# Kernel optimization log

Measured on AMD Instinct MI355X. Metric: run time of the kernel, lower is better.

The kernel has to match this reference:

```python
import jax, jax.numpy as jnp
import numpy as np
from jax import lax

RADIUS = 4
SIGMA_1 = 5.0
SIGMA_2 = 1.0


def _gaussian_kernel_3d(radius, sigma):
    x = np.linspace(-radius, radius, 2 * radius + 1)
    xx, yy, zz = np.meshgrid(x, x, x)
    dist2 = xx ** 2 + yy ** 2 + zz ** 2
    k = np.exp(-dist2 / (2.0 * sigma ** 2)).astype(np.float32)
    return jnp.asarray(k)[None, None]  # [O=1, I=1, D, H, W]


def _conv3d_same(x, kernel, radius):
    # x: [B,1,D,H,W], kernel: [1,1,kd,kh,kw]
    pad = [(radius, radius)] * 3
    return lax.conv_general_dilated(
        x, kernel, window_strides=(1, 1, 1), padding=pad,
        dimension_numbers=('NCDHW', 'OIDHW', 'NCDHW'))


def setup_inputs() -> dict:
    key = jax.random.key(0)
    k1, k2 = jax.random.split(key)
    labels = jax.random.uniform(k1, (4, 1, 160, 160, 160), dtype=jnp.float32)
    inputs = jax.random.uniform(k2, (4, 1, 160, 160, 160), dtype=jnp.float32)
    return {"labels": labels, "inputs": inputs}


def reference(labels, inputs):
    kernel = _gaussian_kernel_3d(RADIUS, SIGMA_1)
    num_classes = 2
    p0 = labels[:, 0:1]  # [B,1,D,H,W]
    loss = jnp.float32(0.0)
    for k in range(num_classes):
        class_probs = p0 if k == 0 else 1.0 - p0
        class_mean = (jnp.mean(inputs * class_probs, axis=(2, 3, 4), keepdims=True)
                      / (jnp.mean(class_probs, axis=(2, 3, 4), keepdims=True) + 1e-5))
        diff = jnp.sum((inputs - class_mean) ** 2, axis=1, keepdims=True)  # [B,1,D,H,W]
        weights = jnp.exp(-(diff ** 2) / (SIGMA_2 ** 2))
        numerator = jnp.sum(class_probs * _conv3d_same(class_probs * weights, kernel, RADIUS))
        denominator = jnp.sum(class_probs * _conv3d_same(weights, kernel, RADIUS))
        # L1Loss(scalar, 0) == abs(scalar)
        loss = loss + jnp.abs(numerator / (denominator + 1e-6))
    return jnp.float32(num_classes) - loss
```

## Files before the change

### kernel.cpp

```cpp
#include <hip/hip_runtime.h>
#include <hip/hip_fp16.h>
#include <math.h>

#define NX   160
#define N2   25600
#define N3   4096000
#define NB   4

#define YCH  10
#define NBLK_XY 1600
#define ZSLAB 20

#define ZCH  20
#define NBLK_Z 800

__device__ __constant__ float G1[9] = {
    0.72614903f, 0.83527021f, 0.92311635f, 0.98019867f, 1.0f,
    0.98019867f, 0.92311635f, 0.83527021f, 0.72614903f};

#define ES_FULL 7.92946852f
__device__ __constant__ float ES_M[4] = {3.46473426f, 2.48453559f, 1.56141924f,
                                         0.72614903f};
__device__ inline float edge_sum(int i) {
    float s = ES_FULL;
    if (i < 4) s -= ES_M[i];
    if (i > NX - 5) s -= ES_M[NX - 1 - i];
    return s;
}

__device__ inline float4 f4_zero() { return make_float4(0.f, 0.f, 0.f, 0.f); }
__device__ inline float4 f4_axpy(float a, float4 b, float4 c) {
    return make_float4(c.x + a * b.x, c.y + a * b.y, c.z + a * b.z, c.w + a * b.w);
}

__device__ inline float4 load_t4(const __half* p) {
    uint2 u = *(const uint2*)p;
    __half2 a = *(const __half2*)&u.x;
    __half2 b = *(const __half2*)&u.y;
    float2 fa = __half22float2(a);
    float2 fb = __half22float2(b);
    return make_float4(fa.x, fa.y, fb.x, fb.y);
}

template <int NV>
__device__ inline void block_reduce_store(double* vals, double* dst) {
    __shared__ double red[4][NV];
    int lane = threadIdx.x & 63;
    int wave = threadIdx.x >> 6;
#pragma unroll
    for (int v = 0; v < NV; ++v) {
        double x = vals[v];
#pragma unroll
        for (int off = 32; off > 0; off >>= 1) x += __shfl_down(x, off, 64);
        if (lane == 0) red[wave][v] = x;
    }
    __syncthreads();
    if (threadIdx.x < NV) {
        int v = threadIdx.x;
        dst[v] = red[0][v] + red[1][v] + red[2][v] + red[3][v];
    }
}

__global__ __launch_bounds__(256) void conv_xy_kernel(
    const float* __restrict__ labels, const float* __restrict__ inputs,
    __half* __restrict__ t, double* __restrict__ pS) {
    int tid = threadIdx.x;
    int xcd = blockIdx.x & 7;
    int v   = blockIdx.x >> 3;
    int idx = v * 256 + tid;
    int x4  = idx % 40;
    int rest = idx / 40;
    int yc  = rest % 16;
    int zb  = rest / 16;
    int z   = (zb % ZSLAB) + ZSLAB * xcd;
    int b   = zb / ZSLAB;

    int x0 = x4 * 4;
    int y0 = yc * YCH;
    const float* plane = labels + b * N3 + z * N2;
    const float* iplane = inputs + b * N3 + z * N2;
    __half* tplane = t + b * N3 + z * N2;

    float4 win[9];
#pragma unroll
    for (int d = 0; d < 9; ++d) {
        int gy = y0 - 4 + d;
        bool rowok = (gy >= 0) && (gy < NX);
        float w[12];
#pragma unroll
        for (int c = 0; c < 3; ++c) {
            int gx = x0 - 4 + 4 * c;
            float4 vv = (rowok && gx >= 0 && gx <= NX - 4)
                            ? *(const float4*)&plane[gy * NX + gx]
                            : f4_zero();
            w[4 * c] = vv.x; w[4 * c + 1] = vv.y;
            w[4 * c + 2] = vv.z; w[4 * c + 3] = vv.w;
        }
        float4 o = f4_zero();
#pragma unroll
        for (int k = 0; k < 9; ++k) {
            float g = G1[k];
            o.x += g * w[k];     o.y += g * w[k + 1];
            o.z += g * w[k + 2]; o.w += g * w[k + 3];
        }
        win[d] = o;
    }

    double sp = 0.0, sip = 0.0, si = 0.0;
#pragma unroll 2
    for (int yo = 0; yo < YCH; ++yo) {
        int y = y0 + yo;
        int gy = y + 5;
        bool rowok = (gy < NX) && (yo < YCH - 1);
        float w[12];
#pragma unroll
        for (int c = 0; c < 3; ++c) {
            int gx = x0 - 4 + 4 * c;
            float4 vv = (rowok && gx >= 0 && gx <= NX - 4)
                            ? *(const float4*)&plane[gy * NX + gx]
                            : f4_zero();
            w[4 * c] = vv.x; w[4 * c + 1] = vv.y;
            w[4 * c + 2] = vv.z; w[4 * c + 3] = vv.w;
        }
        int go = y * NX + x0;
        float4 p = *(const float4*)&plane[go];
        float4 in = *(const float4*)&iplane[go];
        float4 acc = f4_zero();
#pragma unroll
        for (int d = 0; d < 9; ++d) acc = f4_axpy(G1[d], win[d], acc);
        __half2 ha = __floats2half2_rn(acc.x, acc.y);
        __half2 hb = __floats2half2_rn(acc.z, acc.w);
        uint2 u;
        u.x = *(unsigned int*)&ha;
        u.y = *(unsigned int*)&hb;
        *(uint2*)&tplane[go] = u;
        sp += (double)(p.x + p.y + p.z + p.w);
        sip += (double)(in.x * p.x + in.y * p.y + in.z * p.z + in.w * p.w);
        si += (double)(in.x + in.y + in.z + in.w);
        float4 o = f4_zero();
#pragma unroll
        for (int k = 0; k < 9; ++k) {
            float g = G1[k];
            o.x += g * w[k];     o.y += g * w[k + 1];
            o.z += g * w[k + 2]; o.w += g * w[k + 3];
        }
#pragma unroll
        for (int d = 0; d < 8; ++d) win[d] = win[d + 1];
        win[8] = o;
    }
    double vals[3] = {sp, sip, si};
    block_reduce_store<3>(vals, pS + 3 * blockIdx.x);
}

__global__ __launch_bounds__(256) void conv_z_kernel(
    const __half* __restrict__ t, const float* __restrict__ labels,
    const float* __restrict__ inputs, const double* __restrict__ pS,
    double* __restrict__ pZ) {
    int tid = threadIdx.x;
    int xcd = blockIdx.x & 7;
    int c   = blockIdx.x >> 3;
    int idx = c * 256 + tid;
    int x4 = idx % 40;
    int rest = idx / 40;
    int y = rest % NX;
    int b = rest / NX;
    int z0 = ZSLAB * xcd;

    __shared__ float sM[2];
    {
        double v0 = 0, v1 = 0, v2 = 0;
        for (int i = tid; i < 400; i += 256) {
            const double* p = pS + 3 * (400 * b + i);
            v0 += p[0]; v1 += p[1]; v2 += p[2];
        }
        __shared__ double red[4][3];
        int lane = tid & 63, wave = tid >> 6;
        double vals[3] = {v0, v1, v2};
#pragma unroll
        for (int v = 0; v < 3; ++v) {
            double x = vals[v];
#pragma unroll
            for (int off = 32; off > 0; off >>= 1) x += __shfl_down(x, off, 64);
            if (lane == 0) red[wave][v] = x;
        }
        __syncthreads();
        if (tid == 0) {
            double sp = red[0][0] + red[1][0] + red[2][0] + red[3][0];
            double sip = red[0][1] + red[1][1] + red[2][1] + red[3][1];
            double si = red[0][2] + red[1][2] + red[2][2] + red[3][2];
            const double Nv = (double)N3;
            sM[0] = (float)((sip / Nv) / (sp / Nv + 1e-5));
            sM[1] = (float)(((si - sip) / Nv) / ((Nv - sp) / Nv + 1e-5));
        }
        __syncthreads();
    }
    float m0 = sM[0], m1 = sM[1];

    int x = x4 * 4;
    float ey = edge_sum(y);
    float cx[4] = {edge_sum(x) * ey, edge_sum(x + 1) * ey,
                   edge_sum(x + 2) * ey, edge_sum(x + 3) * ey};

    int base = b * N3 + y * NX + x;

    float4 win[9];
#pragma unroll
    for (int d = 0; d < 9; ++d) {
        int z = z0 - 4 + d;
        win[d] = (z >= 0 && z < NX) ? load_t4(&t[base + z * N2]) : f4_zero();
    }

    float n0 = 0.f, d0 = 0.f, n1 = 0.f, d1 = 0.f;
    for (int zb5 = 0; zb5 < 5; ++zb5) {
        int z = z0 + 4 * zb5;
        float4 tn[4], pv[4], iv[4];
#pragma unroll
        for (int j = 0; j < 4; ++j) {
            int zl = z + j + 5;
            tn[j] = (zl < NX) ? load_t4(&t[base + zl * N2]) : f4_zero();
            int gi = base + (z + j) * N2;
            pv[j] = *(const float4*)&labels[gi];
            iv[j] = *(const float4*)&inputs[gi];
        }
#pragma unroll
        for (int j = 0; j < 4; ++j) {
            float4 c4 = f4_zero();
#pragma unroll
            for (int d = 0; d < 9; ++d) c4 = f4_axpy(G1[d], win[d], c4);
            float ez = edge_sum(z + j);
            float pc[4] = {pv[j].x, pv[j].y, pv[j].z, pv[j].w};
            float ic[4] = {iv[j].x, iv[j].y, iv[j].z, iv[j].w};
            float cc[4] = {c4.x, c4.y, c4.z, c4.w};
#pragma unroll
            for (int l = 0; l < 4; ++l) {
                float c1 = cx[l] * ez - cc[l];
                float df0 = ic[l] - m0; df0 *= df0;
                float w0 = __expf(-df0 * df0);
                float df1 = ic[l] - m1; df1 *= df1;
                float w1 = __expf(-df1 * df1);
                n0 += cc[l] * pc[l] * w0;
                d0 += cc[l] * w0;
                n1 += c1 * (1.f - pc[l]) * w1;
                d1 += c1 * w1;
            }
#pragma unroll
            for (int d = 0; d < 8; ++d) win[d] = win[d + 1];
            win[8] = tn[j];
        }
    }
    double vals[4] = {(double)n0, (double)d0, (double)n1, (double)d1};
    block_reduce_store<4>(vals, pZ + 4 * blockIdx.x);
}

__global__ __launch_bounds__(256) void finalize_kernel(
    const double* __restrict__ pZ, float* __restrict__ out) {
    double a0 = 0, a1 = 0, a2 = 0, a3 = 0;
    for (int i = threadIdx.x; i < NBLK_Z; i += 256) {
        const double* p = &pZ[4 * i];
        a0 += p[0]; a1 += p[1]; a2 += p[2]; a3 += p[3];
    }
    __shared__ double red[4][4];
    int lane = threadIdx.x & 63;
    int wave = threadIdx.x >> 6;
    double vals[4] = {a0, a1, a2, a3};
#pragma unroll
    for (int v = 0; v < 4; ++v) {
        double x = vals[v];
#pragma unroll
        for (int off = 32; off > 0; off >>= 1) x += __shfl_down(x, off, 64);
        if (lane == 0) red[wave][v] = x;
    }
    __syncthreads();
    if (threadIdx.x == 0) {
        double acc[4];
#pragma unroll
        for (int v = 0; v < 4; ++v)
            acc[v] = red[0][v] + red[1][v] + red[2][v] + red[3][v];
        double r0 = fabs(acc[0] / (acc[1] + 1e-6));
        double r1 = fabs(acc[2] / (acc[3] + 1e-6));
        out[0] = (float)(2.0 - r0 - r1);
    }
}

extern "C" void kernel_launch(void* const* d_in, const int* in_sizes, int n_in,
                              void* d_out, int out_size, void* d_ws, size_t ws_size,
                              hipStream_t stream) {
    const float* labels = (const float*)d_in[0];
    const float* inputs = (const float*)d_in[1];
    float* out = (float*)d_out;

    double* pS = (double*)d_ws;
    double* pZ = (double*)((char*)d_ws + 192128);
    __half* t  = (__half*)((char*)d_ws + 524288);

    hipLaunchKernelGGL(conv_xy_kernel, dim3(NBLK_XY), dim3(256), 0, stream,
                       labels, inputs, t, pS);
    hipLaunchKernelGGL(conv_z_kernel, dim3(NBLK_Z), dim3(256), 0, stream,
                       t, labels, inputs, pS, pZ);
    hipLaunchKernelGGL(finalize_kernel, dim3(1), dim3(256), 0, stream, pZ, out);
}
```

Before: 196.5 us.

## Fuse xy and z convolution passes, recomputing xy conv per plane

Removes the fp16 intermediate buffer written by the xy-convolution pass. The z-convolution kernel now recomputes the full 9x9 xy convolution for every plane it slides over, reading labels directly. The class-mean sums move into a separate streaming kernel over contiguous chunks. This avoids the intermediate write and read traffic and the fp16 rounding. In exchange, each thread does far more global/cache loads and FMAs per plane, with only 800 blocks to hide that latency.

```diff
diff --git a/kernel.cpp b/kernel.cpp
--- a/kernel.cpp
+++ b/kernel.cpp
@@ -1,5 +1,4 @@
 #include <hip/hip_runtime.h>
-#include <hip/hip_fp16.h>
 #include <math.h>
 
 #define NX   160
@@ -7,10 +6,10 @@
 #define N3   4096000
 #define NB   4
 
-#define YCH  10
-#define NBLK_XY 1600
 #define ZSLAB 20
-
+#define NBLK_S 2048
+#define SBLK_PER_B 512
+#define F4_PER_BLK 2000
 #define ZCH  20
 #define NBLK_Z 800
 
@@ -33,13 +32,33 @@
     return make_float4(c.x + a * b.x, c.y + a * b.y, c.z + a * b.z, c.w + a * b.w);
 }
 
-__device__ inline float4 load_t4(const __half* p) {
-    uint2 u = *(const uint2*)p;
-    __half2 a = *(const __half2*)&u.x;
-    __half2 b = *(const __half2*)&u.y;
-    float2 fa = __half22float2(a);
-    float2 fb = __half22float2(b);
-    return make_float4(fa.x, fa.y, fb.x, fb.y);
+__device__ inline float4 xyconv4(const float* __restrict__ plane, int x0, int y) {
+    float4 acc = f4_zero();
+#pragma unroll
+    for (int dy = 0; dy < 9; ++dy) {
+        int gy = y - 4 + dy;
+        if (gy >= 0 && gy < NX) {
+            const float* row = plane + gy * NX;
+            float w[12];
+#pragma unroll
+            for (int c = 0; c < 3; ++c) {
+                int gx = x0 - 4 + 4 * c;
+                float4 v = (gx >= 0 && gx <= NX - 4) ? *(const float4*)&row[gx]
+                                                     : f4_zero();
+                w[4 * c] = v.x; w[4 * c + 1] = v.y;
+                w[4 * c + 2] = v.z; w[4 * c + 3] = v.w;
+            }
+            float4 o = f4_zero();
+#pragma unroll
+            for (int k = 0; k < 9; ++k) {
+                float g = G1[k];
+                o.x += g * w[k];     o.y += g * w[k + 1];
+                o.z += g * w[k + 2]; o.w += g * w[k + 3];
+            }
+            acc = f4_axpy(G1[dy], o, acc);
+        }
+    }
+    return acc;
 }
 
 template <int NV>
@@ -61,104 +80,32 @@
     }
 }
 
-__global__ __launch_bounds__(256) void conv_xy_kernel(
+__global__ __launch_bounds__(256) void sums_kernel(
     const float* __restrict__ labels, const float* __restrict__ inputs,
-    __half* __restrict__ t, double* __restrict__ pS) {
-    int tid = threadIdx.x;
-    int xcd = blockIdx.x & 7;
-    int v   = blockIdx.x >> 3;
-    int idx = v * 256 + tid;
-    int x4  = idx % 40;
-    int rest = idx / 40;
-    int yc  = rest % 16;
-    int zb  = rest / 16;
-    int z   = (zb % ZSLAB) + ZSLAB * xcd;
-    int b   = zb / ZSLAB;
-
-    int x0 = x4 * 4;
-    int y0 = yc * YCH;
-    const float* plane = labels + b * N3 + z * N2;
-    const float* iplane = inputs + b * N3 + z * N2;
-    __half* tplane = t + b * N3 + z * N2;
-
-    float4 win[9];
-#pragma unroll
-    for (int d = 0; d < 9; ++d) {
-        int gy = y0 - 4 + d;
-        bool rowok = (gy >= 0) && (gy < NX);
-        float w[12];
-#pragma unroll
-        for (int c = 0; c < 3; ++c) {
-            int gx = x0 - 4 + 4 * c;
-            float4 vv = (rowok && gx >= 0 && gx <= NX - 4)
-                            ? *(const float4*)&plane[gy * NX + gx]
-                            : f4_zero();
-            w[4 * c] = vv.x; w[4 * c + 1] = vv.y;
-            w[4 * c + 2] = vv.z; w[4 * c + 3] = vv.w;
-        }
-        float4 o = f4_zero();
-#pragma unroll
-        for (int k = 0; k < 9; ++k) {
-            float g = G1[k];
-            o.x += g * w[k];     o.y += g * w[k + 1];
-            o.z += g * w[k + 2]; o.w += g * w[k + 3];
-        }
-        win[d] = o;
-    }
-
+    double* __restrict__ pS) {
+    int blk = blockIdx.x;
+    int b = blk >> 9;
+    int chunk = blk & 511;
+    const float4* lp = (const float4*)(labels + b * N3) + chunk * F4_PER_BLK;
+    const float4* ip = (const float4*)(inputs + b * N3) + chunk * F4_PER_BLK;
     double sp = 0.0, sip = 0.0, si = 0.0;
-#pragma unroll 2
-    for (int yo = 0; yo < YCH; ++yo) {
-        int y = y0 + yo;
-        int gy = y + 5;
-        bool rowok = (gy < NX) && (yo < YCH - 1);
-        float w[12];
-#pragma unroll
-        for (int c = 0; c < 3; ++c) {
-            int gx = x0 - 4 + 4 * c;
-            float4 vv = (rowok && gx >= 0 && gx <= NX - 4)
-                            ? *(const float4*)&plane[gy * NX + gx]
-                            : f4_zero();
-            w[4 * c] = vv.x; w[4 * c + 1] = vv.y;
-            w[4 * c + 2] = vv.z; w[4 * c + 3] = vv.w;
-        }
-        int go = y * NX + x0;
-        float4 p = *(const float4*)&plane[go];
-        float4 in = *(const float4*)&iplane[go];
-        float4 acc = f4_zero();
-#pragma unroll
-        for (int d = 0; d < 9; ++d) acc = f4_axpy(G1[d], win[d], acc);
-        __half2 ha = __floats2half2_rn(acc.x, acc.y);
-        __half2 hb = __floats2half2_rn(acc.z, acc.w);
-        uint2 u;
-        u.x = *(unsigned int*)&ha;
-        u.y = *(unsigned int*)&hb;
-        *(uint2*)&tplane[go] = u;
+    for (int i = threadIdx.x; i < F4_PER_BLK; i += 256) {
+        float4 p = lp[i];
+        float4 in = ip[i];
         sp += (double)(p.x + p.y + p.z + p.w);
         sip += (double)(in.x * p.x + in.y * p.y + in.z * p.z + in.w * p.w);
         si += (double)(in.x + in.y + in.z + in.w);
-        float4 o = f4_zero();
-#pragma unroll
-        for (int k = 0; k < 9; ++k) {
-            float g = G1[k];
-            o.x += g * w[k];     o.y += g * w[k + 1];
-            o.z += g * w[k + 2]; o.w += g * w[k + 3];
-        }
-#pragma unroll
-        for (int d = 0; d < 8; ++d) win[d] = win[d + 1];
-        win[8] = o;
     }
     double vals[3] = {sp, sip, si};
-    block_reduce_store<3>(vals, pS + 3 * blockIdx.x);
-}
-
-__global__ __launch_bounds__(256) void conv_z_kernel(
-    const __half* __restrict__ t, const float* __restrict__ labels,
-    const float* __restrict__ inputs, const double* __restrict__ pS,
-    double* __restrict__ pZ) {
+    block_reduce_store<3>(vals, pS + 3 * blk);
+}
+
+__global__ __launch_bounds__(256) void fused_conv_kernel(
+    const float* __restrict__ labels, const float* __restrict__ inputs,
+    const double* __restrict__ pS, double* __restrict__ pZ) {
     int tid = threadIdx.x;
     int xcd = blockIdx.x & 7;
-    int c   = blockIdx.x >> 3;
+    int c = blockIdx.x >> 3;
     int idx = c * 256 + tid;
     int x4 = idx % 40;
     int rest = idx / 40;
@@ -169,8 +116,8 @@
     __shared__ float sM[2];
     {
         double v0 = 0, v1 = 0, v2 = 0;
-        for (int i = tid; i < 400; i += 256) {
-            const double* p = pS + 3 * (400 * b + i);
+        for (int i = tid; i < SBLK_PER_B; i += 256) {
+            const double* p = pS + 3 * (SBLK_PER_B * b + i);
             v0 += p[0]; v1 += p[1]; v2 += p[2];
         }
         __shared__ double red[4][3];
@@ -201,52 +148,47 @@
     float cx[4] = {edge_sum(x) * ey, edge_sum(x + 1) * ey,
                    edge_sum(x + 2) * ey, edge_sum(x + 3) * ey};
 
-    int base = b * N3 + y * NX + x;
+    const float* lbase = labels + b * N3;
+    const float* ibase = inputs + b * N3;
+    int po = y * NX + x;
 
     float4 win[9];
 #pragma unroll
     for (int d = 0; d < 9; ++d) {
         int z = z0 - 4 + d;
-        win[d] = (z >= 0 && z < NX) ? load_t4(&t[base + z * N2]) : f4_zero();
+        win[d] = (z >= 0 && z < NX) ? xyconv4(lbase + z * N2, x, y) : f4_zero();
     }
 
     float n0 = 0.f, d0 = 0.f, n1 = 0.f, d1 = 0.f;
-    for (int zb5 = 0; zb5 < 5; ++zb5) {
-        int z = z0 + 4 * zb5;
-        float4 tn[4], pv[4], iv[4];
-#pragma unroll
-        for (int j = 0; j < 4; ++j) {
-            int zl = z + j + 5;
-            tn[j] = (zl < NX) ? load_t4(&t[base + zl * N2]) : f4_zero();
-            int gi = base + (z + j) * N2;
-            pv[j] = *(const float4*)&labels[gi];
-            iv[j] = *(const float4*)&inputs[gi];
-        }
-#pragma unroll
-        for (int j = 0; j < 4; ++j) {
-            float4 c4 = f4_zero();
-#pragma unroll
-            for (int d = 0; d < 9; ++d) c4 = f4_axpy(G1[d], win[d], c4);
-            float ez = edge_sum(z + j);
-            float pc[4] = {pv[j].x, pv[j].y, pv[j].z, pv[j].w};
-            float ic[4] = {iv[j].x, iv[j].y, iv[j].z, iv[j].w};
-            float cc[4] = {c4.x, c4.y, c4.z, c4.w};
-#pragma unroll
-            for (int l = 0; l < 4; ++l) {
-                float c1 = cx[l] * ez - cc[l];
-                float df0 = ic[l] - m0; df0 *= df0;
-                float w0 = __expf(-df0 * df0);
-                float df1 = ic[l] - m1; df1 *= df1;
-                float w1 = __expf(-df1 * df1);
-                n0 += cc[l] * pc[l] * w0;
-                d0 += cc[l] * w0;
-                n1 += c1 * (1.f - pc[l]) * w1;
-                d1 += c1 * w1;
-            }
-#pragma unroll
-            for (int d = 0; d < 8; ++d) win[d] = win[d + 1];
-            win[8] = tn[j];
-        }
+    for (int zz = 0; zz < ZCH; ++zz) {
+        int z = z0 + zz;
+        int zl = z + 5;
+        float4 tn = (zl < NX) ? xyconv4(lbase + zl * N2, x, y) : f4_zero();
+        float4 pv = *(const float4*)&lbase[z * N2 + po];
+        float4 iv = *(const float4*)&ibase[z * N2 + po];
+
+        float4 c4 = f4_zero();
+#pragma unroll
+        for (int d = 0; d < 9; ++d) c4 = f4_axpy(G1[d], win[d], c4);
+        float ez = edge_sum(z);
+        float pc[4] = {pv.x, pv.y, pv.z, pv.w};
+        float ic[4] = {iv.x, iv.y, iv.z, iv.w};
+        float cc[4] = {c4.x, c4.y, c4.z, c4.w};
+#pragma unroll
+        for (int l = 0; l < 4; ++l) {
+            float c1 = cx[l] * ez - cc[l];
+            float df0 = ic[l] - m0; df0 *= df0;
+            float w0 = __expf(-df0 * df0);
+            float df1 = ic[l] - m1; df1 *= df1;
+            float w1 = __expf(-df1 * df1);
+            n0 += cc[l] * pc[l] * w0;
+            d0 += cc[l] * w0;
+            n1 += c1 * (1.f - pc[l]) * w1;
+            d1 += c1 * w1;
+        }
+#pragma unroll
+        for (int d = 0; d < 8; ++d) win[d] = win[d + 1];
+        win[8] = tn;
     }
     double vals[4] = {(double)n0, (double)d0, (double)n1, (double)d1};
     block_reduce_store<4>(vals, pZ + 4 * blockIdx.x);
@@ -291,11 +233,10 @@
 
     double* pS = (double*)d_ws;
     double* pZ = (double*)((char*)d_ws + 192128);
-    __half* t  = (__half*)((char*)d_ws + 524288);
-
-    hipLaunchKernelGGL(conv_xy_kernel, dim3(NBLK_XY), dim3(256), 0, stream,
-                       labels, inputs, t, pS);
-    hipLaunchKernelGGL(conv_z_kernel, dim3(NBLK_Z), dim3(256), 0, stream,
-                       t, labels, inputs, pS, pZ);
+
+    hipLaunchKernelGGL(sums_kernel, dim3(NBLK_S), dim3(256), 0, stream,
+                       labels, inputs, pS);
+    hipLaunchKernelGGL(fused_conv_kernel, dim3(NBLK_Z), dim3(256), 0, stream,
+                       labels, inputs, pS, pZ);
     hipLaunchKernelGGL(finalize_kernel, dim3(1), dim3(256), 0, stream, pZ, out);
 }
```

Result: slower. 316.6 us (+61.2%).
